# Optimization experiments

Hardware: AMD Instinct MI355X
Metric: run time of the kernel (lower is better)

Reference implementation:

```python
import jax, jax.numpy as jnp
import numpy as np

B, N, D, S, H = 128, 4096, 64, 7, 128  # batch, tokens, slot_size, num_slots, mlp_hidden
EPS = 1e-8
LN_EPS = 1e-5


def _ln(x, w, b):
    m = jnp.mean(x, axis=-1, keepdims=True)
    v = jnp.mean((x - m) ** 2, axis=-1, keepdims=True)
    return (x - m) * jax.lax.rsqrt(v + LN_EPS) * w + b


def setup_inputs() -> dict:
    key = jax.random.key(0)
    ks = jax.random.split(key, 12)
    glorot = lambda k, shape: jax.random.normal(k, shape, jnp.float32) * (2.0 / sum(shape)) ** 0.5
    return {
        "inputs": jax.random.normal(ks[0], (B, N, D), jnp.float32),
        "slots_noise": jax.random.normal(ks[1], (B, S, D), jnp.float32),
        "ln_in_w": jnp.ones((D,), jnp.float32), "ln_in_b": jnp.zeros((D,), jnp.float32),
        "ln_slots_w": jnp.ones((D,), jnp.float32), "ln_slots_b": jnp.zeros((D,), jnp.float32),
        "ln_mlp_w": jnp.ones((D,), jnp.float32), "ln_mlp_b": jnp.zeros((D,), jnp.float32),
        "slots_mu": jax.random.normal(ks[2], (1, 1, D), jnp.float32),
        "slots_log_sigma": jax.random.normal(ks[3], (1, 1, D), jnp.float32) * 0.1,
        "Wq": glorot(ks[4], (D, D)), "Wk": glorot(ks[5], (D, D)), "Wv": glorot(ks[6], (D, D)),
        "W_ih": glorot(ks[7], (3 * D, D)), "W_hh": glorot(ks[8], (3 * D, D)),
        "b_ih": jnp.zeros((3 * D,), jnp.float32), "b_hh": jnp.zeros((3 * D,), jnp.float32),
        "mlp_W1": glorot(ks[9], (H, D)), "mlp_b1": jnp.zeros((H,), jnp.float32),
        "mlp_W2": glorot(ks[10], (D, H)), "mlp_b2": jnp.zeros((D,), jnp.float32),
        "num_iterations": 3,
    }


def reference(inputs, slots_noise, ln_in_w, ln_in_b, ln_slots_w, ln_slots_b,
              ln_mlp_w, ln_mlp_b, slots_mu, slots_log_sigma, Wq, Wk, Wv,
              W_ih, W_hh, b_ih, b_hh, mlp_W1, mlp_b1, mlp_W2, mlp_b2,
              num_iterations):
    d = inputs.shape[-1]
    x = _ln(inputs, ln_in_w, ln_in_b)            # [B,N,D]
    k = x @ Wk.T                                  # [B,N,D]
    v = x @ Wv.T                                  # [B,N,D]
    slots = slots_mu + jnp.exp(slots_log_sigma) * slots_noise  # [B,S,D]
    scale = d ** -0.5
    for _ in range(num_iterations):
        slots_prev = slots
        s = _ln(slots, ln_slots_w, ln_slots_b)
        q = (s @ Wq.T) * scale                    # [B,S,D]
        logits = jnp.einsum('bnd,bsd->bns', k, q) # [B,N,S]
        attn = jax.nn.softmax(logits, axis=-1) + EPS   # softmax over slots
        attn = attn / jnp.sum(attn, axis=-2, keepdims=True)  # renorm over tokens
        updates = jnp.einsum('bns,bnd->bsd', attn, v)  # [B,S,D]
        # GRUCell (torch semantics)
        gi = updates @ W_ih.T + b_ih              # [B,S,3D]
        gh = slots_prev @ W_hh.T + b_hh
        i_r, i_z, i_n = jnp.split(gi, 3, axis=-1)
        h_r, h_z, h_n = jnp.split(gh, 3, axis=-1)
        r = jax.nn.sigmoid(i_r + h_r)
        z = jax.nn.sigmoid(i_z + h_z)
        n = jnp.tanh(i_n + r * h_n)
        slots = (1.0 - z) * n + z * slots_prev
        m = _ln(slots, ln_mlp_w, ln_mlp_b)
        slots = slots + (jax.nn.relu(m @ mlp_W1.T + mlp_b1) @ mlp_W2.T + mlp_b2)
    return slots
```

## Files before the change

### kernel.cpp

```cpp
#include <hip/hip_runtime.h>


#define Nn 4096

typedef _Float16 f16;
typedef _Float16 f16x8 __attribute__((ext_vector_type(8)));
typedef _Float16 f16x4 __attribute__((ext_vector_type(4)));
typedef float    f32x4 __attribute__((ext_vector_type(4)));

#define MFMA16(a,b,c) __builtin_amdgcn_mfma_f32_16x16x16f16(a,b,c,0,0,0)
#define MFMA32(a,b,c) __builtin_amdgcn_mfma_f32_16x16x32_f16(a,b,c,0,0,0)
#define LGKM0() asm volatile("s_waitcnt lgkmcnt(0)" ::: "memory")

#if __has_builtin(__builtin_amdgcn_rcpf)
#define RCPF(x) __builtin_amdgcn_rcpf(x)
#else
#define RCPF(x) (1.0f/(x))
#endif

static __device__ __forceinline__ float dot4(f32x4 a, f32x4 b) {
  return a.x*b.x + a.y*b.y + a.z*b.z + a.w*b.w;
}

__global__ __launch_bounds__(256) void k_init(
    const float* __restrict__ noise, const float* __restrict__ mu,
    const float* __restrict__ ls, const float* __restrict__ Wq,
    const float* __restrict__ Wk, float* __restrict__ slots,
    float* __restrict__ Mt)
{
  int bk = blockIdx.x, t = threadIdx.x;
  if (bk < 56) {
    int i = bk*1024 + t*4;
    int d = i & 63;
    f32x4 nz = *(const f32x4*)(noise + i);
    f32x4 m4 = *(const f32x4*)(mu + d);
    f32x4 l4 = *(const f32x4*)(ls + d);
    f32x4 o;
    o.x = m4.x + expf(l4.x)*nz.x; o.y = m4.y + expf(l4.y)*nz.y;
    o.z = m4.z + expf(l4.z)*nz.z; o.w = m4.w + expf(l4.w)*nz.w;
    *(f32x4*)(slots + i) = o;
  } else {
    int idx = (bk-56)*256 + t;
    int d = idx >> 6, e = idx & 63;
    float a = 0.f;
    for (int dd = 0; dd < 64; dd++)
      a += Wk[dd*64 + d] * Wq[dd*64 + e];
    Mt[idx] = a * 0.125f;
  }
}

static __device__ __forceinline__ void stage_chunk(
    float (*Wl)[68], const float* __restrict__ src, int stride, int t)
{
  __syncthreads();
  int r = t >> 2, c4 = (t & 3) * 16;
  #pragma unroll
  for (int k = 0; k < 4; k++)
    *(f32x4*)&Wl[r][c4 + k*4] = *(const f32x4*)(src + (size_t)r*stride + c4 + k*4);
  __syncthreads();
}

static __device__ __forceinline__ float dot_row(
    float (*Wl)[68], int d, const float* v)
{
  float a = 0.f;
  #pragma unroll
  for (int jc = 0; jc < 16; jc++)
    a += dot4(*(const f32x4*)&Wl[d][jc*4], *(const f32x4*)(v + jc*4));
  return a;
}

__global__ __launch_bounds__(256) void k_gru(
    const float* __restrict__ part, const float* __restrict__ csp,
    const float* __restrict__ lnw_in, const float* __restrict__ lnb_in,
    const float* __restrict__ Wv,
    const float* __restrict__ W_ih, const float* __restrict__ W_hh,
    const float* __restrict__ b_ih, const float* __restrict__ b_hh,
    const float* __restrict__ lnm_w, const float* __restrict__ lnm_b,
    const float* __restrict__ W1, const float* __restrict__ b1,
    const float* __restrict__ W2, const float* __restrict__ b2,
    const float* __restrict__ lns_w, const float* __restrict__ lns_b,
    const float* __restrict__ Mt,
    float* __restrict__ slots, f16* __restrict__ qkpad,
    float* __restrict__ qkaux, int do_gru, int do_q)
{
  __shared__ __align__(16) float Wl[64][68];
  __shared__ __align__(16) float updv[4][64];
  __shared__ __align__(16) float u2v [4][64];
  __shared__ __align__(16) float prevv[4][64];
  __shared__ __align__(16) float mlnv[4][64];
  __shared__ __align__(16) float sn2 [4][64];
  __shared__ __align__(16) float hbuf[4][128];
  const int t = threadIdx.x, w = t >> 6, d = t & 63;
  const int wid = blockIdx.x*4 + w;
  const int b = wid / 7, s = wid - b*7;

  float out;
  if (do_gru) {
    float Y = 0.f, alpha = 0.f;
    #pragma unroll
    for (int cx = 0; cx < 8; cx++) {
      Y     += part[(((size_t)b*8+cx)*8 + s)*64 + d];
      alpha += csp [(((size_t)b*8+cx)*8 + s)];
    }
    float upd_pre = lnw_in[d]*(Y/alpha) + lnb_in[d];
    float prev = slots[(size_t)wid*64 + d];
    updv[w][d] = upd_pre; prevv[w][d] = prev;
    LGKM0();

    stage_chunk(Wl, Wv, 64, t);
    u2v[w][d] = dot_row(Wl, d, updv[w]);
    LGKM0();

    stage_chunk(Wl, W_ih,         64, t);
    float air = b_ih[d]     + dot_row(Wl, d, u2v[w]);
    stage_chunk(Wl, W_ih + 4096,  64, t);
    float aiz = b_ih[64+d]  + dot_row(Wl, d, u2v[w]);
    stage_chunk(Wl, W_ih + 8192,  64, t);
    float ain = b_ih[128+d] + dot_row(Wl, d, u2v[w]);
    stage_chunk(Wl, W_hh,         64, t);
    float ahr = b_hh[d]     + dot_row(Wl, d, prevv[w]);
    stage_chunk(Wl, W_hh + 4096,  64, t);
    float ahz = b_hh[64+d]  + dot_row(Wl, d, prevv[w]);
    stage_chunk(Wl, W_hh + 8192,  64, t);
    float ahn = b_hh[128+d] + dot_row(Wl, d, prevv[w]);

    float r = 1.f/(1.f + __expf(-(air+ahr)));
    float z = 1.f/(1.f + __expf(-(aiz+ahz)));
    float n = tanhf(ain + r*ahn);
    float hnew = (1.f - z)*n + z*prev;

    float s1 = hnew, s2 = hnew*hnew;
    #pragma unroll
    for (int m = 1; m < 64; m <<= 1) {
      s1 += __shfl_xor(s1, m, 64);
      s2 += __shfl_xor(s2, m, 64);
    }
    float mean = s1*(1.f/64.f), var = s2*(1.f/64.f) - mean*mean;
    float mln = (hnew - mean) * rsqrtf(var + 1e-5f) * lnm_w[d] + lnm_b[d];
    mlnv[w][d] = mln;
    LGKM0();

    stage_chunk(Wl, W1,        64, t);
    float h0 = fmaxf(b1[d]    + dot_row(Wl, d, mlnv[w]), 0.f);
    stage_chunk(Wl, W1 + 4096, 64, t);
    float h1 = fmaxf(b1[64+d] + dot_row(Wl, d, mlnv[w]), 0.f);
    hbuf[w][d] = h0; hbuf[w][64+d] = h1;
    LGKM0();

    stage_chunk(Wl, W2,      128, t);
    out = hnew + b2[d] + dot_row(Wl, d, hbuf[w]);
    stage_chunk(Wl, W2 + 64, 128, t);
    out += dot_row(Wl, d, hbuf[w] + 64);
    slots[(size_t)wid*64 + d] = out;
  } else {
    out = slots[(size_t)wid*64 + d];
  }

  if (do_q) {
    float s1 = out, s2 = out*out;
    #pragma unroll
    for (int m = 1; m < 64; m <<= 1) {
      s1 += __shfl_xor(s1, m, 64);
      s2 += __shfl_xor(s2, m, 64);
    }
    float mean = s1*(1.f/64.f), var = s2*(1.f/64.f) - mean*mean;
    float sv = (out - mean) * rsqrtf(var + 1e-5f) * lns_w[d] + lns_b[d];
    sn2[w][d] = sv;
    LGKM0();

    stage_chunk(Wl, Mt, 64, t);
    float qk = dot_row(Wl, d, sn2[w]);

    float qw = qk * lnw_in[d];
    float bb = qk * lnb_in[d];
    #pragma unroll
    for (int m = 1; m < 64; m <<= 1)
      bb += __shfl_xor(bb, m, 64);
    qkpad[((size_t)b*16 + s)*64 + d] = (f16)qw;
    if (d == 0) qkaux[(size_t)b*16 + s] = bb;
  }
}

static __device__ __forceinline__ void tile_common(
    f16x8 xf0, f16x8 xf1, const f16x8* qkB, float beta,
    f16x8 selLo, f16x8 selHi, bool valid, f32x4* acc, float& csump)
{
  const f32x4 zero4 = {0.f,0.f,0.f,0.f};
  f32x4 lg = zero4;
  lg = MFMA32(xf0, qkB[0], lg);
  lg = MFMA32(xf1, qkB[1], lg);
  float e[4], sm[4];
  #pragma unroll
  for (int j = 0; j < 4; j++) {
    float L = lg[j] + beta;
    e[j] = valid ? __expf(L) : 0.f;
    sm[j] = e[j];
  }
  #pragma unroll
  for (int m = 1; m < 16; m <<= 1)
    #pragma unroll
    for (int j = 0; j < 4; j++) sm[j] += __shfl_xor(sm[j], m, 64);
  f16x4 pp;
  #pragma unroll
  for (int j = 0; j < 4; j++) {
    float p = valid ? (e[j]*RCPF(sm[j]) + 1e-8f) : 0.f;
    csump += p;
    pp[j] = (f16)p;
  }
  #pragma unroll
  for (int nb = 0; nb < 4; nb++) {
    f32x4 tr = MFMA32(nb < 2 ? xf0 : xf1, (nb & 1) ? selHi : selLo, zero4);
    f16x4 xt; xt.x=(f16)tr.x; xt.y=(f16)tr.y; xt.z=(f16)tr.z; xt.w=(f16)tr.w;
    acc[nb] = MFMA16(pp, xt, acc[nb]);
  }
}

__global__ __launch_bounds__(256, 4) void k_attn(
    const float* __restrict__ x_in, const f16* __restrict__ qkpad,
    const float* __restrict__ qkaux, f16* __restrict__ xh,
    float* __restrict__ part, float* __restrict__ csp, int first)
{
  __shared__ __align__(16) float accb[4][8][64];
  __shared__ float ldsc[4][8];
  const int b = blockIdx.y, cx = blockIdx.x;
  const int tid = threadIdx.x;
  const int w = tid >> 6, lane = tid & 63, q = lane >> 4, c = lane & 15;

  f16x8 qkB[2];
  qkB[0] = *(const f16x8*)(qkpad + ((size_t)b*16 + c)*64 + q*8);
  qkB[1] = *(const f16x8*)(qkpad + ((size_t)b*16 + c)*64 + 32 + q*8);
  const float beta = qkaux[(size_t)b*16 + c];

  f16x8 selLo, selHi;
  #pragma unroll
  for (int j = 0; j < 8; j++) {
    selLo[j] = (f16)((( c>>3)    == q && (c&7) == j) ? 1.0f : 0.0f);
    selHi[j] = (f16)(((c>>3) + 2 == q && (c&7) == j) ? 1.0f : 0.0f);
  }

  const f32x4 zero4 = {0.f,0.f,0.f,0.f};
  f32x4 acc[4] = {zero4, zero4, zero4, zero4};
  float csump = 0.f;
  const size_t tok0 = (size_t)b*Nn + (size_t)cx*512 + (size_t)w*128;
  const bool valid = (c < 7);

  if (first) {
    f32x4 nx[4];
    {
      const float* base = x_in + (tok0 + c)*64;
      nx[0] = *(const f32x4*)(base + q*8);
      nx[1] = *(const f32x4*)(base + q*8 + 4);
      nx[2] = *(const f32x4*)(base + 32 + q*8);
      nx[3] = *(const f32x4*)(base + 32 + q*8 + 4);
    }
    #pragma unroll
    for (int t = 0; t < 8; t++) {
      f32x4 xv[4];
      #pragma unroll
      for (int i = 0; i < 4; i++) xv[i] = nx[i];
      if (t < 7) {
        const float* base = x_in + (tok0 + (t+1)*16 + c)*64;
        nx[0] = *(const f32x4*)(base + q*8);
        nx[1] = *(const f32x4*)(base + q*8 + 4);
        nx[2] = *(const f32x4*)(base + 32 + q*8);
        nx[3] = *(const f32x4*)(base + 32 + q*8 + 4);
      }
      float sx  = (xv[0].x+xv[0].y+xv[0].z+xv[0].w) + (xv[1].x+xv[1].y+xv[1].z+xv[1].w)
                + (xv[2].x+xv[2].y+xv[2].z+xv[2].w) + (xv[3].x+xv[3].y+xv[3].z+xv[3].w);
      float sxx = dot4(xv[0],xv[0]) + dot4(xv[1],xv[1])
                + dot4(xv[2],xv[2]) + dot4(xv[3],xv[3]);
      sx  += __shfl_xor(sx, 16, 64);  sx  += __shfl_xor(sx, 32, 64);
      sxx += __shfl_xor(sxx, 16, 64); sxx += __shfl_xor(sxx, 32, 64);
      float mean = sx*(1.f/64.f);
      float rstd = rsqrtf(sxx*(1.f/64.f) - mean*mean + 1e-5f);
      float mr2 = mean * rstd;
      f16x8 xf0, xf1;
      #pragma unroll
      for (int j = 0; j < 4; j++) {
        xf0[j]   = (f16)(xv[0][j]*rstd - mr2);
        xf0[4+j] = (f16)(xv[1][j]*rstd - mr2);
        xf1[j]   = (f16)(xv[2][j]*rstd - mr2);
        xf1[4+j] = (f16)(xv[3][j]*rstd - mr2);
      }
      f16* xo = xh + (tok0 + t*16 + c)*64;
      *(f16x8*)(xo + q*8)      = xf0;
      *(f16x8*)(xo + 32 + q*8) = xf1;

      tile_common(xf0, xf1, qkB, beta, selLo, selHi, valid, acc, csump);
    }
  } else {
    f16x8 n0, n1;
    {
      const f16* base = xh + (tok0 + c)*64;
      n0 = *(const f16x8*)(base + q*8);
      n1 = *(const f16x8*)(base + 32 + q*8);
    }
    #pragma unroll
    for (int t = 0; t < 8; t++) {
      f16x8 xf0 = n0, xf1 = n1;
      if (t < 7) {
        const f16* base = xh + (tok0 + (t+1)*16 + c)*64;
        n0 = *(const f16x8*)(base + q*8);
        n1 = *(const f16x8*)(base + 32 + q*8);
      }
      tile_common(xf0, xf1, qkB, beta, selLo, selHi, valid, acc, csump);
    }
  }

  csump += __shfl_xor(csump, 16, 64); csump += __shfl_xor(csump, 32, 64);
  if (q == 0 && c < 7) ldsc[w][c] = csump;
  if (q < 2) {
    #pragma unroll
    for (int nb = 0; nb < 4; nb++)
      #pragma unroll
      for (int r = 0; r < 4; r++)
        accb[w][q*4 + r][nb*16 + c] = acc[nb][r];
  }
  __syncthreads();
  for (int rr = tid; rr < 448; rr += 256) {
    int row = rr >> 6, dd = rr & 63;
    float v = accb[0][row][dd] + accb[1][row][dd]
            + accb[2][row][dd] + accb[3][row][dd];
    part[(((size_t)b*8 + cx)*8 + row)*64 + dd] = v;
  }
  if (tid < 7) {
    csp[(((size_t)b*8 + cx)*8 + tid)] =
        ldsc[0][tid] + ldsc[1][tid] + ldsc[2][tid] + ldsc[3][tid];
  }
}

extern "C" void kernel_launch(void* const* d_in, const int* in_sizes, int n_in,
                              void* d_out, int out_size, void* d_ws, size_t ws_size,
                              hipStream_t stream) {
  const float* inputs  = (const float*)d_in[0];
  const float* noise   = (const float*)d_in[1];
  const float* ln_in_w = (const float*)d_in[2];
  const float* ln_in_b = (const float*)d_in[3];
  const float* ln_sl_w = (const float*)d_in[4];
  const float* ln_sl_b = (const float*)d_in[5];
  const float* ln_ml_w = (const float*)d_in[6];
  const float* ln_ml_b = (const float*)d_in[7];
  const float* mu   = (const float*)d_in[8];
  const float* ls   = (const float*)d_in[9];
  const float* Wq   = (const float*)d_in[10];
  const float* Wk   = (const float*)d_in[11];
  const float* Wv   = (const float*)d_in[12];
  const float* W_ih = (const float*)d_in[13];
  const float* W_hh = (const float*)d_in[14];
  const float* b_ih = (const float*)d_in[15];
  const float* b_hh = (const float*)d_in[16];
  const float* W1 = (const float*)d_in[17];
  const float* b1 = (const float*)d_in[18];
  const float* W2 = (const float*)d_in[19];
  const float* b2 = (const float*)d_in[20];

  float* slots = (float*)d_out;

  const size_t PART_OFF = 0;
  const size_t CSP_OFF  = PART_OFF + 2097152;
  const size_t QK_OFF   = CSP_OFF  + 32768;
  const size_t QA_OFF   = QK_OFF   + 262144;
  const size_t MT_OFF   = QA_OFF   + 8192;
  const size_t XH_OFF   = MT_OFF   + 16384;
  const size_t NEED     = XH_OFF   + 67108864;
  if (ws_size < NEED) return;

  char* ws = (char*)d_ws;
  float* part  = (float*)(ws + PART_OFF);
  float* csp   = (float*)(ws + CSP_OFF);
  f16*   qkpad = (f16*)  (ws + QK_OFF);
  float* qkaux = (float*)(ws + QA_OFF);
  float* Mt    = (float*)(ws + MT_OFF);
  f16*   xh    = (f16*)  (ws + XH_OFF);

  k_init<<<72, 256, 0, stream>>>(noise, mu, ls, Wq, Wk, slots, Mt);
  k_gru<<<224, 256, 0, stream>>>(part, csp, ln_in_w, ln_in_b, Wv,
                                 W_ih, W_hh, b_ih, b_hh, ln_ml_w, ln_ml_b,
                                 W1, b1, W2, b2, ln_sl_w, ln_sl_b, Mt,
                                 slots, qkpad, qkaux, 0, 1);
  dim3 ga(8, 128);
  for (int it = 0; it < 3; it++) {
    k_attn<<<ga, 256, 0, stream>>>(inputs, qkpad, qkaux, xh, part, csp,
                                   it == 0 ? 1 : 0);
    k_gru<<<224, 256, 0, stream>>>(part, csp, ln_in_w, ln_in_b, Wv,
                                   W_ih, W_hh, b_ih, b_hh, ln_ml_w, ln_ml_b,
                                   W1, b1, W2, b2, ln_sl_w, ln_sl_b, Mt,
                                   slots, qkpad, qkaux, 1, it < 2 ? 1 : 0);
  }
}
```

Baseline: 322.3 us.

## Split attention into more token chunks and batch GRU weight staging in LDS

After: 318.0 us. Within noise of the previous version (-1.3%).

```diff
diff --git a/kernel.cpp b/kernel.cpp
--- a/kernel.cpp
+++ b/kernel.cpp
@@ -2,6 +2,7 @@
 
 
 #define Nn 4096
+#define NCH 16
 
 typedef _Float16 f16;
 typedef _Float16 f16x8 __attribute__((ext_vector_type(8)));
@@ -49,25 +50,24 @@
   }
 }
 
-static __device__ __forceinline__ void stage_chunk(
-    float (*Wl)[68], const float* __restrict__ src, int stride, int t)
-{
-  __syncthreads();
-  int r = t >> 2, c4 = (t & 3) * 16;
+static __device__ __forceinline__ void stageN(
+    float (*dst)[68], const float* __restrict__ src, int stride, int sr, int sc)
+{
   #pragma unroll
   for (int k = 0; k < 4; k++)
-    *(f32x4*)&Wl[r][c4 + k*4] = *(const f32x4*)(src + (size_t)r*stride + c4 + k*4);
-  __syncthreads();
+    *(f32x4*)&dst[sr][sc + k*4] = *(const f32x4*)(src + (size_t)sr*stride + sc + k*4);
 }
 
 static __device__ __forceinline__ float dot_row(
-    float (*Wl)[68], int d, const float* v)
-{
-  float a = 0.f;
-  #pragma unroll
-  for (int jc = 0; jc < 16; jc++)
-    a += dot4(*(const f32x4*)&Wl[d][jc*4], *(const f32x4*)(v + jc*4));
-  return a;
+    const float (*Wl)[68], int d, const float* v)
+{
+  float a0 = 0.f, a1 = 0.f;
+  #pragma unroll
+  for (int jc = 0; jc < 16; jc += 2) {
+    a0 += dot4(*(const f32x4*)&Wl[d][jc*4],     *(const f32x4*)(v + jc*4));
+    a1 += dot4(*(const f32x4*)&Wl[d][jc*4 + 4], *(const f32x4*)(v + jc*4 + 4));
+  }
+  return a0 + a1;
 }
 
 __global__ __launch_bounds__(256) void k_gru(
@@ -84,7 +84,7 @@
     float* __restrict__ slots, f16* __restrict__ qkpad,
     float* __restrict__ qkaux, int do_gru, int do_q)
 {
-  __shared__ __align__(16) float Wl[64][68];
+  __shared__ __align__(16) float WA[7][64][68];
   __shared__ __align__(16) float updv[4][64];
   __shared__ __align__(16) float u2v [4][64];
   __shared__ __align__(16) float prevv[4][64];
@@ -94,36 +94,42 @@
   const int t = threadIdx.x, w = t >> 6, d = t & 63;
   const int wid = blockIdx.x*4 + w;
   const int b = wid / 7, s = wid - b*7;
+  const int sr = t >> 2, sc = (t & 3) * 16;
 
   float out;
   if (do_gru) {
+    {
+      const float* srcs[7] = { Wv, W_ih, W_ih + 4096, W_ih + 8192,
+                               W_hh, W_hh + 4096, W_hh + 8192 };
+      #pragma unroll
+      for (int i = 0; i < 7; i++) stageN(WA[i], srcs[i], 64, sr, sc);
+    }
     float Y = 0.f, alpha = 0.f;
     #pragma unroll
-    for (int cx = 0; cx < 8; cx++) {
-      Y     += part[(((size_t)b*8+cx)*8 + s)*64 + d];
-      alpha += csp [(((size_t)b*8+cx)*8 + s)];
+    for (int cx = 0; cx < NCH; cx++) {
+      Y     += part[(((size_t)b*NCH + cx)*8 + s)*64 + d];
+      alpha += csp [ ((size_t)b*NCH + cx)*8 + s];
     }
     float upd_pre = lnw_in[d]*(Y/alpha) + lnb_in[d];
     float prev = slots[(size_t)wid*64 + d];
     updv[w][d] = upd_pre; prevv[w][d] = prev;
+    __syncthreads();
+
+    u2v[w][d] = dot_row(WA[0], d, updv[w]);
     LGKM0();
-
-    stage_chunk(Wl, Wv, 64, t);
-    u2v[w][d] = dot_row(Wl, d, updv[w]);
-    LGKM0();
-
-    stage_chunk(Wl, W_ih,         64, t);
-    float air = b_ih[d]     + dot_row(Wl, d, u2v[w]);
-    stage_chunk(Wl, W_ih + 4096,  64, t);
-    float aiz = b_ih[64+d]  + dot_row(Wl, d, u2v[w]);
-    stage_chunk(Wl, W_ih + 8192,  64, t);
-    float ain = b_ih[128+d] + dot_row(Wl, d, u2v[w]);
-    stage_chunk(Wl, W_hh,         64, t);
-    float ahr = b_hh[d]     + dot_row(Wl, d, prevv[w]);
-    stage_chunk(Wl, W_hh + 4096,  64, t);
-    float ahz = b_hh[64+d]  + dot_row(Wl, d, prevv[w]);
-    stage_chunk(Wl, W_hh + 8192,  64, t);
-    float ahn = b_hh[128+d] + dot_row(Wl, d, prevv[w]);
+    float air = b_ih[d]     + dot_row(WA[1], d, u2v[w]);
+    float aiz = b_ih[64+d]  + dot_row(WA[2], d, u2v[w]);
+    float ain = b_ih[128+d] + dot_row(WA[3], d, u2v[w]);
+    float ahr = b_hh[d]     + dot_row(WA[4], d, prevv[w]);
+    float ahz = b_hh[64+d]  + dot_row(WA[5], d, prevv[w]);
+    float ahn = b_hh[128+d] + dot_row(WA[6], d, prevv[w]);
+    __syncthreads();
+
+    stageN(WA[0], W1,        64,  sr, sc);
+    stageN(WA[1], W1 + 4096, 64,  sr, sc);
+    stageN(WA[2], W2,        128, sr, sc);
+    stageN(WA[3], W2 + 64,   128, sr, sc);
+    stageN(WA[4], Mt,        64,  sr, sc);
 
     float r = 1.f/(1.f + __expf(-(air+ahr)));
     float z = 1.f/(1.f + __expf(-(aiz+ahz)));
@@ -139,22 +145,19 @@
     float mean = s1*(1.f/64.f), var = s2*(1.f/64.f) - mean*mean;
     float mln = (hnew - mean) * rsqrtf(var + 1e-5f) * lnm_w[d] + lnm_b[d];
     mlnv[w][d] = mln;
-    LGKM0();
-
-    stage_chunk(Wl, W1,        64, t);
-    float h0 = fmaxf(b1[d]    + dot_row(Wl, d, mlnv[w]), 0.f);
-    stage_chunk(Wl, W1 + 4096, 64, t);
-    float h1 = fmaxf(b1[64+d] + dot_row(Wl, d, mlnv[w]), 0.f);
+    __syncthreads();
+
+    float h0 = fmaxf(b1[d]    + dot_row(WA[0], d, mlnv[w]), 0.f);
+    float h1 = fmaxf(b1[64+d] + dot_row(WA[1], d, mlnv[w]), 0.f);
     hbuf[w][d] = h0; hbuf[w][64+d] = h1;
     LGKM0();
-
-    stage_chunk(Wl, W2,      128, t);
-    out = hnew + b2[d] + dot_row(Wl, d, hbuf[w]);
-    stage_chunk(Wl, W2 + 64, 128, t);
-    out += dot_row(Wl, d, hbuf[w] + 64);
+    out = hnew + b2[d] + dot_row(WA[2], d, hbuf[w])
+                       + dot_row(WA[3], d, hbuf[w] + 64);
     slots[(size_t)wid*64 + d] = out;
   } else {
+    stageN(WA[4], Mt, 64, sr, sc);
     out = slots[(size_t)wid*64 + d];
+    __syncthreads();
   }
 
   if (do_q) {
@@ -169,8 +172,7 @@
     sn2[w][d] = sv;
     LGKM0();
 
-    stage_chunk(Wl, Mt, 64, t);
-    float qk = dot_row(Wl, d, sn2[w]);
+    float qk = dot_row(WA[4], d, sn2[w]);
 
     float qw = qk * lnw_in[d];
     float bb = qk * lnb_in[d];
@@ -242,7 +244,7 @@
   const f32x4 zero4 = {0.f,0.f,0.f,0.f};
   f32x4 acc[4] = {zero4, zero4, zero4, zero4};
   float csump = 0.f;
-  const size_t tok0 = (size_t)b*Nn + (size_t)cx*512 + (size_t)w*128;
+  const size_t tok0 = (size_t)b*Nn + (size_t)cx*256 + (size_t)w*64;
   const bool valid = (c < 7);
 
   if (first) {
@@ -255,11 +257,11 @@
       nx[3] = *(const f32x4*)(base + 32 + q*8 + 4);
     }
     #pragma unroll
-    for (int t = 0; t < 8; t++) {
+    for (int t = 0; t < 4; t++) {
       f32x4 xv[4];
       #pragma unroll
       for (int i = 0; i < 4; i++) xv[i] = nx[i];
-      if (t < 7) {
+      if (t < 3) {
         const float* base = x_in + (tok0 + (t+1)*16 + c)*64;
         nx[0] = *(const f32x4*)(base + q*8);
         nx[1] = *(const f32x4*)(base + q*8 + 4);
@@ -290,22 +292,16 @@
       tile_common(xf0, xf1, qkB, beta, selLo, selHi, valid, acc, csump);
     }
   } else {
-    f16x8 n0, n1;
-    {
-      const f16* base = xh + (tok0 + c)*64;
-      n0 = *(const f16x8*)(base + q*8);
-      n1 = *(const f16x8*)(base + 32 + q*8);
-    }
-    #pragma unroll
-    for (int t = 0; t < 8; t++) {
-      f16x8 xf0 = n0, xf1 = n1;
-      if (t < 7) {
-        const f16* base = xh + (tok0 + (t+1)*16 + c)*64;
-        n0 = *(const f16x8*)(base + q*8);
-        n1 = *(const f16x8*)(base + 32 + q*8);
-      }
-      tile_common(xf0, xf1, qkB, beta, selLo, selHi, valid, acc, csump);
-    }
+    f16x8 L0[4], L1[4];
+    #pragma unroll
+    for (int t = 0; t < 4; t++) {
+      const f16* base = xh + (tok0 + t*16 + c)*64;
+      L0[t] = *(const f16x8*)(base + q*8);
+      L1[t] = *(const f16x8*)(base + 32 + q*8);
+    }
+    #pragma unroll
+    for (int t = 0; t < 4; t++)
+      tile_common(L0[t], L1[t], qkB, beta, selLo, selHi, valid, acc, csump);
   }
 
   csump += __shfl_xor(csump, 16, 64); csump += __shfl_xor(csump, 32, 64);
@@ -322,10 +318,10 @@
     int row = rr >> 6, dd = rr & 63;
     float v = accb[0][row][dd] + accb[1][row][dd]
             + accb[2][row][dd] + accb[3][row][dd];
-    part[(((size_t)b*8 + cx)*8 + row)*64 + dd] = v;
+    part[(((size_t)b*NCH + cx)*8 + row)*64 + dd] = v;
   }
   if (tid < 7) {
-    csp[(((size_t)b*8 + cx)*8 + tid)] =
+    csp[((size_t)b*NCH + cx)*8 + tid] =
         ldsc[0][tid] + ldsc[1][tid] + ldsc[2][tid] + ldsc[3][tid];
   }
 }
@@ -358,8 +354,8 @@
   float* slots = (float*)d_out;
 
   const size_t PART_OFF = 0;
-  const size_t CSP_OFF  = PART_OFF + 2097152;
-  const size_t QK_OFF   = CSP_OFF  + 32768;
+  const size_t CSP_OFF  = PART_OFF + 4194304;
+  const size_t QK_OFF   = CSP_OFF  + 65536;
   const size_t QA_OFF   = QK_OFF   + 262144;
   const size_t MT_OFF   = QA_OFF   + 8192;
   const size_t XH_OFF   = MT_OFF   + 16384;
@@ -379,7 +375,7 @@
                                  W_ih, W_hh, b_ih, b_hh, ln_ml_w, ln_ml_b,
                                  W1, b1, W2, b2, ln_sl_w, ln_sl_b, Mt,
                                  slots, qkpad, qkaux, 0, 1);
-  dim3 ga(8, 128);
+  dim3 ga(NCH, 128);
   for (int it = 0; it < 3; it++) {
     k_attn<<<ga, 256, 0, stream>>>(inputs, qkpad, qkaux, xh, part, csp,
                                    it == 0 ? 1 : 0);
```
